# Kernel optimization log

Hardware: AMD Instinct MI355X
Metric: run time of the kernel (lower is better)

The kernel has to match this reference:

```python
import jax, jax.numpy as jnp
from jax import lax
import numpy as np

F = 64          # filters
KH = KW = 3     # kernel size
STRIDE = 16     # input conv stride


def setup_inputs() -> dict:
    key = jax.random.key(0)
    k1, k2, k3, k4 = jax.random.split(key, 4)
    B, T, H, W, C = 16, 8, 256, 256, 3
    x = jax.random.normal(k1, (B, T, H, W, C), dtype=jnp.float32)
    # Keras ConvLSTM2D fuses the 4 gates (i, f, c, o) along output channels.
    Wx = jax.random.normal(k2, (KH, KW, C, 4 * F), dtype=jnp.float32) * 0.05
    Wh = jax.random.normal(k3, (KH, KW, F, 4 * F), dtype=jnp.float32) * 0.05
    b = jax.random.normal(k4, (4 * F,), dtype=jnp.float32) * 0.05
    return {"x": x, "Wx": Wx, "Wh": Wh, "b": b}


def _conv(inp, kern, strides):
    return lax.conv_general_dilated(
        inp, kern, window_strides=strides, padding="SAME",
        dimension_numbers=("NHWC", "HWIO", "NHWC"))


def _hard_sigmoid(z):
    # Keras ConvLSTM2D default recurrent_activation
    return jnp.clip(0.2 * z + 0.5, 0.0, 1.0)


def reference(x, Wx, Wh, b):
    B, T, H, W, C = x.shape
    # Strided input conv for all timesteps at once: (B*T,H,W,C) -> (B*T,Ho,Wo,4F)
    xc = _conv(x.reshape(B * T, H, W, C), Wx, (STRIDE, STRIDE))
    Ho, Wo = xc.shape[1], xc.shape[2]
    xc = (xc + b).reshape(B, T, Ho, Wo, 4 * F).transpose(1, 0, 2, 3, 4)  # (T,B,Ho,Wo,4F)

    def step(carry, xt):
        h, c = carry
        z = xt + _conv(h, Wh, (1, 1))          # (B,Ho,Wo,4F)
        zi, zf, zg, zo = jnp.split(z, 4, axis=-1)
        i = _hard_sigmoid(zi)
        f = _hard_sigmoid(zf)
        c = f * c + i * zg                     # activation=None -> linear g
        o = _hard_sigmoid(zo)
        h = o * c                              # activation=None -> linear cell output
        return (h, c), None

    h0 = jnp.zeros((B, Ho, Wo, F), dtype=x.dtype)
    c0 = jnp.zeros((B, Ho, Wo, F), dtype=x.dtype)
    (h, _), _ = lax.scan(step, (h0, c0), xc)
    return h  # return_sequences=False -> last hidden state (B,Ho,Wo,F)
```

## Files before the change

### kernel.cpp

```cpp
#include <hip/hip_runtime.h>

#define NB   16
#define NT   8
#define HIN  256
#define CIN  3
#define NF   64
#define OC   256
#define HO   16
#define WOUT 16

typedef short short8 __attribute__((ext_vector_type(8)));
typedef float f32x16 __attribute__((ext_vector_type(16)));

__device__ __forceinline__ unsigned short f2bf(float x) {
  union { float f; unsigned int u; } v; v.f = x;
  unsigned int r = v.u + 0x7fffu + ((v.u >> 16) & 1u);
  return (unsigned short)(r >> 16);
}

__global__ __launch_bounds__(256) void input_conv(
    const float* __restrict__ x, const float* __restrict__ Wx,
    const float* __restrict__ bias, float* __restrict__ xc)
{
  const int ho = blockIdx.x;
  const int bt = blockIdx.y;
  const int oc = threadIdx.x;

  __shared__ float patch[3 * 16 * 12];
  for (int idx = threadIdx.x; idx < 432; idx += 256) {
    int r = idx / 144, rem = idx % 144;
    int wo = rem / 9, k = rem % 9;
    int kw = k / 3, c = k % 3;
    patch[(r * 16 + wo) * 12 + k] =
        x[(((size_t)bt * HIN + (ho * 16 + r)) * HIN + (wo * 16 + kw)) * CIN + c];
  }
  float w[27];
#pragma unroll
  for (int k = 0; k < 27; ++k) w[k] = Wx[(size_t)k * OC + oc];
  __syncthreads();

  const float bv = bias[oc];
  const int n = (oc & 63) * 4 + (oc >> 6);
  for (int wo = 0; wo < 16; ++wo) {
    float acc = bv;
#pragma unroll
    for (int kh = 0; kh < 3; ++kh) {
      const float* pp = &patch[(kh * 16 + wo) * 12];
      float4 p0 = *(const float4*)pp;
      float4 p1 = *(const float4*)(pp + 4);
      float p8 = pp[8];
      const float* wk = &w[kh * 9];
      acc = fmaf(p0.x, wk[0], fmaf(p0.y, wk[1], fmaf(p0.z, wk[2], acc)));
      acc = fmaf(p0.w, wk[3], fmaf(p1.x, wk[4], fmaf(p1.y, wk[5], acc)));
      acc = fmaf(p1.z, wk[6], fmaf(p1.w, wk[7], fmaf(p8, wk[8], acc)));
    }
    xc[(((size_t)bt * HO + ho) * WOUT + wo) * OC + n] = acc;
  }
}

__global__ __launch_bounds__(256) void conv_weights(
    const float* __restrict__ Wh, unsigned short* __restrict__ Bp)
{
  __shared__ float wt[64 * 256];
  const int tap = blockIdx.x;
  const int t = threadIdx.x;
#pragma unroll
  for (int i = 0; i < 16; ++i) {
    int chunk = t + i * 256;
    *(float4*)&wt[chunk * 4] = *(const float4*)&Wh[(size_t)tap * 16384 + chunk * 4];
  }
  __syncthreads();
#pragma unroll
  for (int rep = 0; rep < 8; ++rep) {
    int u = t + rep * 256;
    int nb = u >> 8, q = (u >> 6) & 3, l = u & 63;
    int n = nb * 32 + (l & 31);
    int oc = (n & 3) * 64 + (n >> 2);
    int ci0 = q * 16 + (l >> 5) * 8;
    short8 v;
#pragma unroll
    for (int j = 0; j < 8; ++j) v[j] = (short)f2bf(wt[(ci0 + j) * 256 + oc]);
    *(short8*)&Bp[(size_t)((nb * 36 + tap * 4 + q) * 64 + l) * 8] = v;
  }
}

#define A_BYTES 23040
#define B_BYTES 36864
__global__ __launch_bounds__(512, 2) void lstm_step(
    const float* __restrict__ xc, const unsigned short* __restrict__ Bp,
    const unsigned short* __restrict__ h_in, unsigned short* __restrict__ h_out,
    float* __restrict__ c_st, float* __restrict__ out,
    int t, int first, int last)
{
  const int mb  = blockIdx.x;
  const int nb  = blockIdx.y;
  const int b   = mb >> 1;
  const int ho0 = (mb & 1) * 8;
  const int tid = threadIdx.x;
  const int w    = tid >> 6;
  const int lane = tid & 63;
  const int mf = w >> 1, kk = w & 1;

  __shared__ __align__(16) char smem[A_BYTES + B_BYTES];
  unsigned short* Bs = (unsigned short*)(smem + A_BYTES);
  float* zs = (float*)smem;

  f32x16 acc = (f32x16)(0.0f);

  if (!first) {
    for (int j = tid; j < 1440; j += 512) {
      int cell = j >> 3, sub = j & 7;
      int r = cell / 18, c = cell - r * 18;
      int y = ho0 + r - 1, xcol = c - 1;
      float4 v = make_float4(0.f, 0.f, 0.f, 0.f);
      if ((unsigned)y < 16u && (unsigned)xcol < 16u)
        v = *(const float4*)(h_in + (((size_t)b * 256 + y * 16 + xcol) * 64 + sub * 8));
      int byte = (cell * 128 + sub * 16) ^ ((cell & 7) << 4);
      *(float4*)(smem + byte) = v;
    }
    for (int j = tid; j < 2304; j += 512)
      *(float4*)((char*)Bs + j * 16) = *(const float4*)(Bp + (size_t)nb * 18432 + j * 8);
    __syncthreads();

    const int p = mf * 32 + (lane & 31);
    const int cell0 = ((p >> 4) + 1) * 18 + (p & 15) + 1;
    const int cib = (lane >> 5) * 16;

#pragma unroll
    for (int uu = 0; uu < 18; ++uu) {
      const int u = uu * 2 + kk;
      const int tap = u >> 2, q = u & 3;
      const int dy = tap / 3 - 1, dx = tap % 3 - 1;
      const int cell = cell0 + dy * 18 + dx;
      const int abyte = (cell * 128 + q * 32 + cib) ^ ((cell & 7) << 4);
      short8 a  = *(const short8*)(smem + abyte);
      short8 bb = *(const short8*)((const char*)Bs + u * 1024 + lane * 16);
      acc = __builtin_amdgcn_mfma_f32_32x32x16_bf16(a, bb, acc, 0, 0, 0);
    }
    __syncthreads();

    const int col = lane & 31;
#pragma unroll
    for (int rr = 0; rr < 4; ++rr) {
      int posl = mf * 32 + rr * 8 + (lane >> 5) * 4;
      float4 vv = make_float4(acc[rr * 4], acc[rr * 4 + 1], acc[rr * 4 + 2], acc[rr * 4 + 3]);
      *(float4*)&zs[(kk * 32 + col) * 129 + posl] = vv;
    }
  }
  __syncthreads();

  const int pos = tid & 127;
  const int fhalf = tid >> 7;
  const int gpos = ho0 * 16 + pos;
  const float* xcb = xc + ((size_t)(b * NT + t) * 256 + gpos) * 256 + nb * 32;
#pragma unroll
  for (int e = 0; e < 2; ++e) {
    int f = fhalf + e * 4;
    float zq0 = 0.f, zq1 = 0.f, zq2 = 0.f, zq3 = 0.f;
    if (!first) {
      zq0 = zs[(f * 4 + 0) * 129 + pos] + zs[(32 + f * 4 + 0) * 129 + pos];
      zq1 = zs[(f * 4 + 1) * 129 + pos] + zs[(32 + f * 4 + 1) * 129 + pos];
      zq2 = zs[(f * 4 + 2) * 129 + pos] + zs[(32 + f * 4 + 2) * 129 + pos];
      zq3 = zs[(f * 4 + 3) * 129 + pos] + zs[(32 + f * 4 + 3) * 129 + pos];
    }
    float4 xq = *(const float4*)(xcb + f * 4);
    float zi = zq0 + xq.x, zf_ = zq1 + xq.y, zg = zq2 + xq.z, zo = zq3 + xq.w;
    float ig = fminf(fmaxf(fmaf(zi, 0.2f, 0.5f), 0.f), 1.f);
    float fg = fminf(fmaxf(fmaf(zf_, 0.2f, 0.5f), 0.f), 1.f);
    float og = fminf(fmaxf(fmaf(zo, 0.2f, 0.5f), 0.f), 1.f);
    size_t ci = ((size_t)b * 256 + gpos) * 64 + nb * 8 + f;
    float cold = first ? 0.f : c_st[ci];
    float cn = fmaf(fg, cold, ig * zg);
    c_st[ci] = cn;
    float h = og * cn;
    h_out[ci] = f2bf(h);
    if (last) out[ci] = h;
  }
}

extern "C" void kernel_launch(void* const* d_in, const int* in_sizes, int n_in,
                              void* d_out, int out_size, void* d_ws, size_t ws_size,
                              hipStream_t stream) {
  const float* x    = (const float*)d_in[0];
  const float* Wx   = (const float*)d_in[1];
  const float* Wh   = (const float*)d_in[2];
  const float* bias = (const float*)d_in[3];
  float* out = (float*)d_out;

  char* ws = (char*)d_ws;
  float*          xc = (float*)ws;
  unsigned short* Bp = (unsigned short*)(ws + 33554432);
  unsigned short* h0 = (unsigned short*)(ws + 33849344);
  unsigned short* h1 = (unsigned short*)(ws + 34373632);
  float*          cb = (float*)(ws + 34897920);

  input_conv<<<dim3(HO, NB * NT), 256, 0, stream>>>(x, Wx, bias, xc);
  conv_weights<<<9, 256, 0, stream>>>(Wh, Bp);

  for (int t = 0; t < NT; ++t) {
    unsigned short* hin  = (t & 1) ? h1 : h0;
    unsigned short* hout = (t & 1) ? h0 : h1;
    lstm_step<<<dim3(32, 8), 512, 0, stream>>>(
        xc, Bp, hin, hout, cb, out, t, t == 0, t == NT - 1);
  }
}
```

Measured before the change: 214.5 us.

## Fuse all LSTM timesteps into one cooperative kernel with grid sync

Replaces the eight per-timestep lstm_step launches with a single persistent cooperative kernel that loops over timesteps and separates them with grid.sync(). The recurrent weight tile is loaded into shared memory once per block instead of once per step, and the gate epilogue is split into two half passes so the z staging buffer fits in the smaller footprint. The aim is to remove per-launch overhead and repeated weight loads. The cost is grid-wide barriers, and the code falls back to the old launches if the cooperative launch fails.

```diff
diff --git a/kernel.cpp b/kernel.cpp
--- a/kernel.cpp
+++ b/kernel.cpp
@@ -1,4 +1,7 @@
 #include <hip/hip_runtime.h>
+#include <hip/hip_cooperative_groups.h>
+
+namespace cg = cooperative_groups;
 
 #define NB   16
 #define NT   8
@@ -86,6 +89,113 @@
 
 #define A_BYTES 23040
 #define B_BYTES 36864
+
+__global__ __launch_bounds__(512, 2) void lstm_all(
+    const float* __restrict__ xc, const unsigned short* __restrict__ Bp,
+    unsigned short* __restrict__ h0, unsigned short* __restrict__ h1,
+    float* __restrict__ c_st, float* __restrict__ out)
+{
+  cg::grid_group grid = cg::this_grid();
+
+  const int bid = blockIdx.x;
+  const int mb  = bid >> 3;
+  const int nb  = bid & 7;
+  const int b   = mb >> 1;
+  const int ho0 = (mb & 1) * 8;
+  const int tid = threadIdx.x;
+  const int w    = tid >> 6;
+  const int lane = tid & 63;
+  const int mf = w >> 1, kk = w & 1;
+
+  __shared__ __align__(16) char smem[A_BYTES + B_BYTES];
+  unsigned short* Bs = (unsigned short*)(smem + A_BYTES);
+  float* zs = (float*)smem;
+
+  for (int j = tid; j < 2304; j += 512)
+    *(float4*)((char*)Bs + j * 16) = *(const float4*)(Bp + (size_t)nb * 18432 + j * 8);
+  __syncthreads();
+
+  const int p = mf * 32 + (lane & 31);
+  const int cell0 = ((p >> 4) + 1) * 18 + (p & 15) + 1;
+  const int cib = (lane >> 5) * 16;
+
+  for (int t = 0; t < NT; ++t) {
+    const int first = (t == 0), last = (t == NT - 1);
+    const unsigned short* h_in  = (t & 1) ? h1 : h0;
+    unsigned short*       h_out = (t & 1) ? h0 : h1;
+
+    f32x16 acc = (f32x16)(0.0f);
+
+    if (!first) {
+      grid.sync();
+
+      for (int j = tid; j < 1440; j += 512) {
+        int cell = j >> 3, sub = j & 7;
+        int r = cell / 18, c = cell - r * 18;
+        int y = ho0 + r - 1, xcol = c - 1;
+        float4 v = make_float4(0.f, 0.f, 0.f, 0.f);
+        if ((unsigned)y < 16u && (unsigned)xcol < 16u)
+          v = *(const float4*)(h_in + (((size_t)b * 256 + y * 16 + xcol) * 64 + sub * 8));
+        int byte = (cell * 128 + sub * 16) ^ ((cell & 7) << 4);
+        *(float4*)(smem + byte) = v;
+      }
+      __syncthreads();
+
+#pragma unroll
+      for (int uu = 0; uu < 18; ++uu) {
+        const int u = uu * 2 + kk;
+        const int tap = u >> 2, q = u & 3;
+        const int dy = tap / 3 - 1, dx = tap % 3 - 1;
+        const int cell = cell0 + dy * 18 + dx;
+        const int abyte = (cell * 128 + q * 32 + cib) ^ ((cell & 7) << 4);
+        short8 a  = *(const short8*)(smem + abyte);
+        short8 bb = *(const short8*)((const char*)Bs + u * 1024 + lane * 16);
+        acc = __builtin_amdgcn_mfma_f32_32x32x16_bf16(a, bb, acc, 0, 0, 0);
+      }
+      __syncthreads();
+    }
+
+    const int col = lane & 31;
+#pragma unroll
+    for (int hp = 0; hp < 2; ++hp) {
+      if (!first && (mf >> 1) == hp) {
+#pragma unroll
+        for (int rr = 0; rr < 4; ++rr) {
+          int off = (mf & 1) * 32 + rr * 8 + (lane >> 5) * 4;
+          float4 vv = make_float4(acc[rr * 4], acc[rr * 4 + 1],
+                                  acc[rr * 4 + 2], acc[rr * 4 + 3]);
+          *(float4*)&zs[(kk * 32 + col) * 68 + off] = vv;
+        }
+      }
+      __syncthreads();
+
+      const int pos_l = tid & 63;
+      const int fl    = tid >> 6;
+      float z0 = 0.f, z1 = 0.f, z2 = 0.f, z3 = 0.f;
+      if (!first) {
+        z0 = zs[(fl * 4 + 0) * 68 + pos_l] + zs[(32 + fl * 4 + 0) * 68 + pos_l];
+        z1 = zs[(fl * 4 + 1) * 68 + pos_l] + zs[(32 + fl * 4 + 1) * 68 + pos_l];
+        z2 = zs[(fl * 4 + 2) * 68 + pos_l] + zs[(32 + fl * 4 + 2) * 68 + pos_l];
+        z3 = zs[(fl * 4 + 3) * 68 + pos_l] + zs[(32 + fl * 4 + 3) * 68 + pos_l];
+      }
+      const int gpos = ho0 * 16 + hp * 64 + pos_l;
+      const float4 xq = *(const float4*)&xc[(((size_t)(b * NT + t) * 256 + gpos)) * 256 + nb * 32 + fl * 4];
+      float zi = z0 + xq.x, zf_ = z1 + xq.y, zg = z2 + xq.z, zo = z3 + xq.w;
+      float ig = fminf(fmaxf(fmaf(zi, 0.2f, 0.5f), 0.f), 1.f);
+      float fg = fminf(fmaxf(fmaf(zf_, 0.2f, 0.5f), 0.f), 1.f);
+      float og = fminf(fmaxf(fmaf(zo, 0.2f, 0.5f), 0.f), 1.f);
+      size_t ci = ((size_t)b * 256 + gpos) * 64 + nb * 8 + fl;
+      float cold = first ? 0.f : c_st[ci];
+      float cn = fmaf(fg, cold, ig * zg);
+      c_st[ci] = cn;
+      float h = og * cn;
+      h_out[ci] = f2bf(h);
+      if (last) out[ci] = h;
+      __syncthreads();
+    }
+  }
+}
+
 __global__ __launch_bounds__(512, 2) void lstm_step(
     const float* __restrict__ xc, const unsigned short* __restrict__ Bp,
     const unsigned short* __restrict__ h_in, unsigned short* __restrict__ h_out,
@@ -197,10 +307,16 @@
   input_conv<<<dim3(HO, NB * NT), 256, 0, stream>>>(x, Wx, bias, xc);
   conv_weights<<<9, 256, 0, stream>>>(Wh, Bp);
 
-  for (int t = 0; t < NT; ++t) {
-    unsigned short* hin  = (t & 1) ? h1 : h0;
-    unsigned short* hout = (t & 1) ? h0 : h1;
-    lstm_step<<<dim3(32, 8), 512, 0, stream>>>(
-        xc, Bp, hin, hout, cb, out, t, t == 0, t == NT - 1);
-  }
-}
+  void* args[] = { (void*)&xc, (void*)&Bp, (void*)&h0, (void*)&h1,
+                   (void*)&cb, (void*)&out };
+  hipError_t err = hipLaunchCooperativeKernel((const void*)lstm_all, dim3(256),
+                                              dim3(512), args, 0, stream);
+  if (err != hipSuccess) {
+    for (int t = 0; t < NT; ++t) {
+      unsigned short* hin  = (t & 1) ? h1 : h0;
+      unsigned short* hout = (t & 1) ? h0 : h1;
+      lstm_step<<<dim3(32, 8), 512, 0, stream>>>(
+          xc, Bp, hin, hout, cb, out, t, t == 0, t == NT - 1);
+    }
+  }
+}
```

Result: slower. 494.6 us (+130.6%).
